# Optimization experiments

Hardware: AMD Instinct MI355X
Metric: run time of the kernel (lower is better)

The kernel has to match this reference:

```python
import jax, jax.numpy as jnp
import numpy as np

B, C, T = 64, 128, 4096
KNOT = 4  # default knot=4 -> 6 spline knots
SIGMA = 0.2


def setup_inputs() -> dict:
    key = jax.random.key(0)
    k1, k2, k3 = jax.random.split(key, 3)
    x = jax.random.normal(k1, (B, C, T), dtype=jnp.float32)
    # yy ~ N(1.0, sigma) as in GenerateRandomCurves
    yy = 1.0 + SIGMA * jax.random.normal(k2, (B, KNOT + 2, C), dtype=jnp.float32)
    mask_rand = jax.random.uniform(k3, (B, 1, 1), dtype=jnp.float32)
    return {"x": x, "yy": yy, "mask_rand": mask_rand}


def _notaknot_matrix(n, h):
    # Moment (second-derivative) system for a not-a-knot cubic spline on a
    # uniform grid with spacing h (matches scipy.interpolate.CubicSpline default bc).
    A = np.zeros((n, n), dtype=np.float32)
    for i in range(1, n - 1):
        A[i, i - 1] = h / 6.0
        A[i, i] = 2.0 * h / 3.0
        A[i, i + 1] = h / 6.0
    # not-a-knot: third derivative continuous at x1 and x_{n-2}
    A[0, 0], A[0, 1], A[0, 2] = 1.0, -2.0, 1.0
    A[-1, -3], A[-1, -2], A[-1, -1] = 1.0, -2.0, 1.0
    return jnp.asarray(A)


def reference(x, yy, mask_rand):
    Bq, Cq, Tq = x.shape
    n = KNOT + 2
    h = (Tq - 1) / (KNOT + 1)  # uniform knot spacing; knots span [0, T-1]
    A = _notaknot_matrix(n, h)

    # Solve for spline moments M (second derivatives at knots), batched over (B, C).
    rhs_int = (yy[:, 2:, :] - 2.0 * yy[:, 1:-1, :] + yy[:, :-2, :]) / h  # (B, n-2, C)
    z = jnp.zeros((Bq, 1, Cq), yy.dtype)
    rhs = jnp.concatenate([z, rhs_int, z], axis=1)  # (B, n, C)
    M = jnp.linalg.solve(A, rhs)  # (B, n, C)

    # Evaluate the spline at t = 0..T-1 (vectorized over all batch/channel).
    tq = jnp.arange(Tq, dtype=x.dtype)
    idx = jnp.clip(jnp.floor(tq / h).astype(jnp.int32), 0, n - 2)  # (T,)
    xl = idx.astype(x.dtype) * h
    dxl = (tq - xl)[None, :, None]       # t - x_i
    dxr = (xl + h - tq)[None, :, None]   # x_{i+1} - t
    Mi, Mi1 = M[:, idx, :], M[:, idx + 1, :]      # (B, T, C)
    yi, yi1 = yy[:, idx, :], yy[:, idx + 1, :]    # (B, T, C)
    curve = ((Mi * dxr**3 + Mi1 * dxl**3) / (6.0 * h)
             + (yi / h - Mi * h / 6.0) * dxr
             + (yi1 / h - Mi1 * h / 6.0) * dxl)   # (B, T, C)

    # DistortTimesteps: cumulative sum, rescaled so the last step lands on T-1.
    tt = jnp.cumsum(curve, axis=1)
    tt = tt * (Tq - 1) / tt[:, -1:, :]  # (B, T, C)

    # Per-(batch, channel) linear interpolation back onto the regular grid.
    xp = tt.transpose(0, 2, 1).reshape(Bq * Cq, Tq)  # warped timestamps
    fp = x.reshape(Bq * Cq, Tq)                      # channel signals
    x_tw = jax.vmap(lambda a, b: jnp.interp(tq, a, b))(xp, fp)
    x_tw = x_tw.reshape(Bq, Cq, Tq)

    mask = mask_rand < 0.5  # (B,1,1): apply warp with probability p=0.5
    return jnp.where(mask, x_tw, x)
```

## Files before the change

kernel.cpp:

```cpp
#include <hip/hip_runtime.h>

#define BB 64
#define CC 128
#define TT 4096
#define NN 6
#define HH 819.0f

__device__ __forceinline__ int padi(int j) { return j + (j >> 5); }

__global__ __launch_bounds__(256) void timewarp_kernel(
    const float* __restrict__ x,
    const float* __restrict__ yy,
    const float* __restrict__ mask_rand,
    float* __restrict__ out)
{
    const int row = blockIdx.x;
    const int b   = row / CC;
    const int c   = row % CC;
    const int tid = threadIdx.x;

    const float* xrow = x + (size_t)row * TT;
    float* orow       = out + (size_t)row * TT;

    if (!(mask_rand[b] < 0.5f)) {
        const float4* xi = (const float4*)xrow;
        float4* oo = (float4*)orow;
        #pragma unroll
        for (int k = 0; k < 4; ++k) {
            int i = tid + 256 * k;
            oo[i] = xi[i];
        }
        return;
    }

    __shared__ float sh_res[TT + TT / 32];
    __shared__ float sh_wsum[4];
    __shared__ float sh_xf[256];
    __shared__ float sh_ff[256];

    float Mv[NN];
    float y[NN];
    {
        #pragma unroll
        for (int k = 0; k < NN; ++k)
            y[k] = yy[((size_t)b * NN + k) * CC + c];
        float Aug[NN][NN + 1];
        #pragma unroll
        for (int i = 0; i < NN; ++i)
            #pragma unroll
            for (int j = 0; j < NN + 1; ++j)
                Aug[i][j] = 0.0f;
        Aug[0][0] = 1.0f;  Aug[0][1] = -2.0f;  Aug[0][2] = 1.0f;
        Aug[5][3] = 1.0f;  Aug[5][4] = -2.0f;  Aug[5][5] = 1.0f;
        #pragma unroll
        for (int i = 1; i < NN - 1; ++i) {
            Aug[i][i - 1] = HH / 6.0f;
            Aug[i][i]     = 2.0f * HH / 3.0f;
            Aug[i][i + 1] = HH / 6.0f;
            Aug[i][NN]    = (y[i + 1] - 2.0f * y[i] + y[i - 1]) / HH;
        }
        #pragma unroll
        for (int k = 0; k < NN; ++k) {
            float inv = 1.0f / Aug[k][k];
            #pragma unroll
            for (int i = k + 1; i < NN; ++i) {
                float m = Aug[i][k] * inv;
                #pragma unroll
                for (int j = k; j < NN + 1; ++j)
                    Aug[i][j] -= m * Aug[k][j];
            }
        }
        #pragma unroll
        for (int i = NN - 1; i >= 0; --i) {
            float s = Aug[i][NN];
            #pragma unroll
            for (int j = i + 1; j < NN; ++j)
                s -= Aug[i][j] * Mv[j];
            Mv[i] = s / Aug[i][i];
        }
    }

    const int t0 = tid * 16;
    float fpv[17];
    {
        const float4* xi = (const float4*)(xrow + t0);
        #pragma unroll
        for (int k = 0; k < 4; ++k) {
            float4 v = xi[k];
            fpv[4 * k + 0] = v.x; fpv[4 * k + 1] = v.y;
            fpv[4 * k + 2] = v.z; fpv[4 * k + 3] = v.w;
        }
    }

    const float inv6h = 1.0f / (6.0f * HH);
    const float hd6   = HH / 6.0f;
    const float invh  = 1.0f / HH;
    float loc[16];
    float running = 0.0f;
    #pragma unroll
    for (int k = 0; k < 16; ++k) {
        int t = t0 + k;
        int idx = t / 819;
        idx = idx > 4 ? 4 : idx;
        float xl  = (float)idx * HH;
        float ft  = (float)t;
        float dxl = ft - xl;
        float dxr = xl + HH - ft;
        float Mi  = Mv[idx], Mi1 = Mv[idx + 1];
        float yi  = y[idx],  yi1 = y[idx + 1];
        float curve = (Mi * dxr * dxr * dxr + Mi1 * dxl * dxl * dxl) * inv6h
                    + (yi * invh - Mi * hd6) * dxr
                    + (yi1 * invh - Mi1 * hd6) * dxl;
        running += curve;
        loc[k] = running;
    }

    const int lane = tid & 63, wid = tid >> 6;
    float ws = running;
    #pragma unroll
    for (int d = 1; d < 64; d <<= 1) {
        float v = __shfl_up(ws, d, 64);
        if (lane >= d) ws += v;
    }
    if (lane == 63) sh_wsum[wid] = ws;
    __syncthreads();
    float wo = 0.0f, total = 0.0f;
    #pragma unroll
    for (int w = 0; w < 4; ++w) {
        float s = sh_wsum[w];
        total += s;
        if (w < wid) wo += s;
    }
    const float offs  = wo + (ws - running);
    const float scale = 4095.0f / total;

    float xpv[17];
    #pragma unroll
    for (int k = 0; k < 16; ++k)
        xpv[k] = (loc[k] + offs) * scale;

    sh_xf[tid] = xpv[0];
    sh_ff[tid] = fpv[0];
    __syncthreads();
    xpv[16] = (tid < 255) ? sh_xf[tid + 1] : xpv[15];
    fpv[16] = (tid < 255) ? sh_ff[tid + 1] : fpv[15];

    if (tid == 0) {
        int q1 = (int)ceilf(xpv[0]);
        if (q1 > TT) q1 = TT;
        for (int q = 0; q < q1; ++q) sh_res[padi(q)] = fpv[0];
    }
    const int nseg = (tid < 255) ? 16 : 15;
    #pragma unroll
    for (int k = 0; k < 16; ++k) {
        if (k < nseg) {
            float xa = xpv[k],  xb = xpv[k + 1];
            float fa = fpv[k],  fb = fpv[k + 1];
            int qlo = (int)ceilf(xa);  if (qlo < 0) qlo = 0;
            int qhi = (int)ceilf(xb) - 1;  if (qhi > TT - 1) qhi = TT - 1;
            float d = xb - xa;
            float slope = (d > 0.0f) ? (fb - fa) / d : 0.0f;
            for (int q = qlo; q <= qhi; ++q)
                sh_res[padi(q)] = fa + ((float)q - xa) * slope;
        }
    }
    if (tid == 255) {
        int q0 = (int)ceilf(xpv[15]);
        if (q0 < 0) q0 = 0;
        for (int q = q0; q <= TT - 1; ++q) sh_res[padi(q)] = fpv[15];
    }
    __syncthreads();

    float4* oo = (float4*)orow;
    #pragma unroll
    for (int kk = 0; kk < 4; ++kk) {
        int i4 = tid + 256 * kk;
        int fb = 4 * i4;
        int p  = padi(fb);
        float4 v;
        v.x = sh_res[p + 0];
        v.y = sh_res[p + 1];
        v.z = sh_res[p + 2];
        v.w = sh_res[p + 3];
        oo[i4] = v;
    }
}

extern "C" void kernel_launch(void* const* d_in, const int* in_sizes, int n_in,
                              void* d_out, int out_size, void* d_ws, size_t ws_size,
                              hipStream_t stream) {
    const float* x    = (const float*)d_in[0];
    const float* yy   = (const float*)d_in[1];
    const float* mask = (const float*)d_in[2];
    float* out = (float*)d_out;
    timewarp_kernel<<<dim3(BB * CC), dim3(256), 0, stream>>>(x, yy, mask, out);
}
```

Baseline: 235.5 us.

## Replace segment scatter interpolation with per-output binary search gather

Switches the interpolation from each thread scattering its source segments into a shared result buffer to each thread binary-searching the warped timestamps in shared memory for its own output points. Block size goes from 256 to 512 threads with 8 elements per thread, and the per-element spline interval lookup is replaced by two precomputed candidate intervals. The aim is to remove the load imbalance of the scatter loops, including the serial fill by the edge threads, and to avoid dynamic register indexing. In exchange it adds 12 dependent shared-memory reads per search and possible bank conflicts.

```diff
diff --git a/kernel.cpp b/kernel.cpp
--- a/kernel.cpp
+++ b/kernel.cpp
@@ -5,10 +5,10 @@
 #define TT 4096
 #define NN 6
 #define HH 819.0f
-
-__device__ __forceinline__ int padi(int j) { return j + (j >> 5); }
-
-__global__ __launch_bounds__(256) void timewarp_kernel(
+#define NTHR 512
+#define EPT 8
+
+__global__ __launch_bounds__(NTHR) void timewarp_kernel(
     const float* __restrict__ x,
     const float* __restrict__ yy,
     const float* __restrict__ mask_rand,
@@ -25,18 +25,17 @@
     if (!(mask_rand[b] < 0.5f)) {
         const float4* xi = (const float4*)xrow;
         float4* oo = (float4*)orow;
-        #pragma unroll
-        for (int k = 0; k < 4; ++k) {
-            int i = tid + 256 * k;
-            oo[i] = xi[i];
-        }
+        oo[tid]        = xi[tid];
+        oo[tid + NTHR] = xi[tid + NTHR];
         return;
     }
 
-    __shared__ float sh_res[TT + TT / 32];
-    __shared__ float sh_wsum[4];
-    __shared__ float sh_xf[256];
-    __shared__ float sh_ff[256];
+    __shared__ float sh_xp[TT];
+    __shared__ float sh_fp[TT];
+    __shared__ float sh_wsum[NTHR / 64];
+
+    const float4 xv0 = ((const float4*)xrow)[tid];
+    const float4 xv1 = ((const float4*)xrow)[tid + NTHR];
 
     float Mv[NN];
     float y[NN];
@@ -80,34 +79,37 @@
         }
     }
 
-    const int t0 = tid * 16;
-    float fpv[17];
-    {
-        const float4* xi = (const float4*)(xrow + t0);
-        #pragma unroll
-        for (int k = 0; k < 4; ++k) {
-            float4 v = xi[k];
-            fpv[4 * k + 0] = v.x; fpv[4 * k + 1] = v.y;
-            fpv[4 * k + 2] = v.z; fpv[4 * k + 3] = v.w;
-        }
-    }
+    const int t0 = tid * EPT;
+    int idxA = t0 / 819;  if (idxA > 4) idxA = 4;
+    int idxB = idxA + 1;  if (idxB > 4) idxB = 4;
+    float MiA = Mv[0], Mi1A = Mv[1], yiA = y[0], yi1A = y[1];
+    #pragma unroll
+    for (int s = 1; s <= 4; ++s)
+        if (idxA >= s) { MiA = Mv[s]; Mi1A = Mv[s + 1]; yiA = y[s]; yi1A = y[s + 1]; }
+    float MiB = Mv[0], Mi1B = Mv[1], yiB = y[0], yi1B = y[1];
+    #pragma unroll
+    for (int s = 1; s <= 4; ++s)
+        if (idxB >= s) { MiB = Mv[s]; Mi1B = Mv[s + 1]; yiB = y[s]; yi1B = y[s + 1]; }
+    const float tb  = (float)((idxA + 1) * 819);
+    const float xlA = (float)idxA * HH;
+    const float xlB = (float)idxB * HH;
 
     const float inv6h = 1.0f / (6.0f * HH);
     const float hd6   = HH / 6.0f;
     const float invh  = 1.0f / HH;
-    float loc[16];
+    float loc[EPT];
     float running = 0.0f;
     #pragma unroll
-    for (int k = 0; k < 16; ++k) {
-        int t = t0 + k;
-        int idx = t / 819;
-        idx = idx > 4 ? 4 : idx;
-        float xl  = (float)idx * HH;
-        float ft  = (float)t;
+    for (int k = 0; k < EPT; ++k) {
+        float ft  = (float)(t0 + k);
+        bool  inB = ft >= tb;
+        float Mi  = inB ? MiB  : MiA;
+        float Mi1 = inB ? Mi1B : Mi1A;
+        float yi  = inB ? yiB  : yiA;
+        float yi1 = inB ? yi1B : yi1A;
+        float xl  = inB ? xlB  : xlA;
         float dxl = ft - xl;
         float dxr = xl + HH - ft;
-        float Mi  = Mv[idx], Mi1 = Mv[idx + 1];
-        float yi  = y[idx],  yi1 = y[idx + 1];
         float curve = (Mi * dxr * dxr * dxr + Mi1 * dxl * dxl * dxl) * inv6h
                     + (yi * invh - Mi * hd6) * dxr
                     + (yi1 * invh - Mi1 * hd6) * dxl;
@@ -115,6 +117,9 @@
         loc[k] = running;
     }
 
+    ((float4*)sh_fp)[tid]        = xv0;
+    ((float4*)sh_fp)[tid + NTHR] = xv1;
+
     const int lane = tid & 63, wid = tid >> 6;
     float ws = running;
     #pragma unroll
@@ -126,7 +131,7 @@
     __syncthreads();
     float wo = 0.0f, total = 0.0f;
     #pragma unroll
-    for (int w = 0; w < 4; ++w) {
+    for (int w = 0; w < NTHR / 64; ++w) {
         float s = sh_wsum[w];
         total += s;
         if (w < wid) wo += s;
@@ -134,55 +139,54 @@
     const float offs  = wo + (ws - running);
     const float scale = 4095.0f / total;
 
-    float xpv[17];
-    #pragma unroll
-    for (int k = 0; k < 16; ++k)
-        xpv[k] = (loc[k] + offs) * scale;
-
-    sh_xf[tid] = xpv[0];
-    sh_ff[tid] = fpv[0];
+    {
+        float4 a, bq;
+        a.x  = (loc[0] + offs) * scale;  a.y  = (loc[1] + offs) * scale;
+        a.z  = (loc[2] + offs) * scale;  a.w  = (loc[3] + offs) * scale;
+        bq.x = (loc[4] + offs) * scale;  bq.y = (loc[5] + offs) * scale;
+        bq.z = (loc[6] + offs) * scale;  bq.w = (loc[7] + offs) * scale;
+        ((float4*)(sh_xp + t0))[0] = a;
+        ((float4*)(sh_xp + t0))[1] = bq;
+    }
     __syncthreads();
-    xpv[16] = (tid < 255) ? sh_xf[tid + 1] : xpv[15];
-    fpv[16] = (tid < 255) ? sh_ff[tid + 1] : fpv[15];
-
-    if (tid == 0) {
-        int q1 = (int)ceilf(xpv[0]);
-        if (q1 > TT) q1 = TT;
-        for (int q = 0; q < q1; ++q) sh_res[padi(q)] = fpv[0];
-    }
-    const int nseg = (tid < 255) ? 16 : 15;
-    #pragma unroll
-    for (int k = 0; k < 16; ++k) {
-        if (k < nseg) {
-            float xa = xpv[k],  xb = xpv[k + 1];
-            float fa = fpv[k],  fb = fpv[k + 1];
-            int qlo = (int)ceilf(xa);  if (qlo < 0) qlo = 0;
-            int qhi = (int)ceilf(xb) - 1;  if (qhi > TT - 1) qhi = TT - 1;
-            float d = xb - xa;
-            float slope = (d > 0.0f) ? (fb - fa) / d : 0.0f;
-            for (int q = qlo; q <= qhi; ++q)
-                sh_res[padi(q)] = fa + ((float)q - xa) * slope;
-        }
-    }
-    if (tid == 255) {
-        int q0 = (int)ceilf(xpv[15]);
-        if (q0 < 0) q0 = 0;
-        for (int q = q0; q <= TT - 1; ++q) sh_res[padi(q)] = fpv[15];
-    }
-    __syncthreads();
-
-    float4* oo = (float4*)orow;
-    #pragma unroll
-    for (int kk = 0; kk < 4; ++kk) {
-        int i4 = tid + 256 * kk;
-        int fb = 4 * i4;
-        int p  = padi(fb);
-        float4 v;
-        v.x = sh_res[p + 0];
-        v.y = sh_res[p + 1];
-        v.z = sh_res[p + 2];
-        v.w = sh_res[p + 3];
-        oo[i4] = v;
+
+    const int q0a = 4 * tid;
+    const int q0b = 4 * (tid + NTHR);
+    const float fq0a = (float)q0a;
+    const float fq0b = (float)q0b;
+    int j0 = -1, j1 = -1;
+    #pragma unroll
+    for (int step = 2048; step >= 1; step >>= 1) {
+        int n0 = j0 + step;  n0 = (n0 > TT - 1) ? TT - 1 : n0;
+        int n1 = j1 + step;  n1 = (n1 > TT - 1) ? TT - 1 : n1;
+        if (sh_xp[n0] <= fq0a) j0 = n0;
+        if (sh_xp[n1] <= fq0b) j1 = n1;
+    }
+
+    #pragma unroll
+    for (int ch = 0; ch < 2; ++ch) {
+        const int qbase = (ch == 0) ? q0a : q0b;
+        int j = (ch == 0) ? j0 : j1;
+        float r[4];
+        #pragma unroll
+        for (int e = 0; e < 4; ++e) {
+            const float fq = (float)(qbase + e);
+            while (j < TT - 1 && sh_xp[j + 1] <= fq) ++j;
+            float v;
+            if (j < 0) {
+                v = sh_fp[0];
+            } else if (j >= TT - 1) {
+                v = sh_fp[TT - 1];
+            } else {
+                float xa = sh_xp[j], xb = sh_xp[j + 1];
+                float fa = sh_fp[j], fb = sh_fp[j + 1];
+                float d  = xb - xa;
+                v = (d > 0.0f) ? fa + (fq - xa) * (fb - fa) / d : fa;
+            }
+            r[e] = v;
+        }
+        float4 res = make_float4(r[0], r[1], r[2], r[3]);
+        ((float4*)orow)[tid + ch * NTHR] = res;
     }
 }
 
@@ -193,5 +197,5 @@
     const float* yy   = (const float*)d_in[1];
     const float* mask = (const float*)d_in[2];
     float* out = (float*)d_out;
-    timewarp_kernel<<<dim3(BB * CC), dim3(256), 0, stream>>>(x, yy, mask, out);
+    timewarp_kernel<<<dim3(BB * CC), dim3(NTHR), 0, stream>>>(x, yy, mask, out);
 }
```

Measured after the change: 232.8 us. No clear change (-1.2%).
